# Kernel optimization log

Hardware: AMD Instinct MI355X
Metric: run time of the kernel (lower is better)

The kernel has to match this reference:

```python
import jax, jax.numpy as jnp
import numpy as np

TWO_PI = 2.0 * np.pi


def interp_H_circular(coords, signal):
    """Circular linear interpolation over a uniform group grid.
    coords: [M, 1] angles; signal: [K, C]. Returns [M, C]."""
    K = signal.shape[0]
    step = TWO_PI / K
    t = jnp.mod(coords[:, 0], TWO_PI) / step          # [M]
    i0f = jnp.floor(t)
    frac = (t - i0f)[:, None]                          # [M, 1]
    i0 = i0f.astype(jnp.int32) % K
    i1 = (i0 + 1) % K
    return (1.0 - frac) * signal[i0] + frac * signal[i1]


def rotate_grid(angles, grid):
    """angles: [No]; grid: [ks, ks, 2] (x, y). Returns [No, ks, ks, 2]."""
    c, s = jnp.cos(angles), jnp.sin(angles)
    R = jnp.stack([jnp.stack([c, -s], -1), jnp.stack([s, c], -1)], -2)  # [No,2,2]
    return jnp.einsum('nij,hwj->nhwi', R, grid)


def bilinear_sample(img, grid):
    """img: [B, H, W]; grid: [B, h, w, 2] with (x, y) in [-1, 1].
    Zero padding outside, align_corners-style mapping. Returns [B, h, w]."""
    B, H, W = img.shape
    x = (grid[..., 0] + 1.0) * 0.5 * (W - 1)
    y = (grid[..., 1] + 1.0) * 0.5 * (H - 1)
    x0f, y0f = jnp.floor(x), jnp.floor(y)
    wx, wy = x - x0f, y - y0f
    x0, y0 = x0f.astype(jnp.int32), y0f.astype(jnp.int32)
    b = jnp.arange(B)[:, None, None]

    def gather(yy, xx):
        valid = (yy >= 0) & (yy < H) & (xx >= 0) & (xx < W)
        v = img[b, jnp.clip(yy, 0, H - 1), jnp.clip(xx, 0, W - 1)]
        return jnp.where(valid, v, 0.0)

    return ((1 - wy) * (1 - wx) * gather(y0, x0)
            + (1 - wy) * wx * gather(y0, x0 + 1)
            + wy * (1 - wx) * gather(y0 + 1, x0)
            + wy * wx * gather(y0 + 1, x0 + 1))


def setup_inputs() -> dict:
    key = jax.random.key(0)
    k1, k2, k3, k4 = jax.random.split(key, 4)
    O, CIN, K, KS, NI, NO = 512, 512, 16, 7, 16, 16
    in_H = jax.random.uniform(k1, (NI, 1), dtype=jnp.float32) * TWO_PI
    out_H = jax.random.uniform(k2, (NO, 1), dtype=jnp.float32) * TWO_PI
    weight_H = jax.random.normal(k3, (O, CIN, K), dtype=jnp.float32) * 0.05
    weight = jax.random.normal(k4, (O, 1, KS, KS), dtype=jnp.float32) * 0.05
    grid_H = (jnp.arange(K, dtype=jnp.float32) * (TWO_PI / K)).reshape(K, 1)
    lin = jnp.linspace(-1.0, 1.0, KS, dtype=jnp.float32)
    gx, gy = jnp.meshgrid(lin, lin, indexing='xy')
    grid_Rn = jnp.stack([gx, gy], axis=-1)  # [KS, KS, 2]
    mask = jnp.ones((KS, KS), dtype=jnp.float32)
    return {"in_H": in_H, "out_H": out_H, "weight_H": weight_H,
            "weight": weight, "grid_H": grid_H, "grid_Rn": grid_Rn,
            "mask": mask}


def reference(in_H, out_H, weight_H, weight, grid_H, grid_Rn, mask):
    NI, NO = in_H.shape[0], out_H.shape[0]
    O, CIN_G, K = weight_H.shape
    KS = weight.shape[-1]

    out_H_inv = -out_H                                            # inverse_H
    # left_apply_to_H: pairwise group product -> [NI, NO, 1]
    H_prod_H = jnp.mod(in_H[:, None, :] + out_H_inv[None, :, :], TWO_PI)
    # left_apply_to_Rn: rotate spatial grid -> [NO, KS, KS, 2]
    H_prod_Rn = rotate_grid(out_H_inv[:, 0], grid_Rn)

    # interpolate_H over group grid of signal [K, CIN_G*O]
    sig = jnp.transpose(weight_H, (2, 1, 0)).reshape(K, -1)
    wH = interp_H_circular(H_prod_H.reshape(-1, 1), sig)          # [NI*NO, CIN_G*O]
    wH = wH.reshape(NI, NO, CIN_G, O)
    # .transpose(0,3).transpose(1,3) == permutation (3,0,2,1)
    weight_H_out = jnp.transpose(wH, (3, 0, 2, 1))                # [O, NI, CIN_G, NO]

    # interpolate_Rn: repeat_interleave kernels, tile rotated grids
    imgs = jnp.repeat(weight[:, 0], NO, axis=0)                   # [O*NO, KS, KS]
    grids = jnp.tile(H_prod_Rn, (O, 1, 1, 1))                     # [O*NO, KS, KS, 2]
    w = bilinear_sample(imgs, grids).reshape(O, NO, 1, KS, KS)
    w = mask * w                                                  # broadcast mask
    return (weight_H_out, w)
```

## Files before the change

### kernel.cpp

```cpp
#include <hip/hip_runtime.h>

#define TWO_PI_F 6.283185307179586f

#define C_O   512
#define C_CIN 512
#define C_K   16
#define C_KS  7
#define C_NI  16
#define C_NO  16

#define OUT0_SIZE (C_O * C_NI * C_CIN * C_NO)
#define OUT1_SIZE (C_O * C_NO * C_KS * C_KS)

#define SW_STRIDE 18

#define BILIN_PER_BLOCK 784

typedef float f32x4 __attribute__((ext_vector_type(4)));

__global__ __launch_bounds__(1024, 8) void fused_kernel(
    const float* __restrict__ in_H,
    const float* __restrict__ out_H,
    const float* __restrict__ weight_H,
    const float* __restrict__ weight,
    const float* __restrict__ grid_Rn,
    const float* __restrict__ mask,
    float* __restrict__ out0,
    float* __restrict__ out1)
{
    __shared__ float s_w[C_CIN * SW_STRIDE];
    __shared__ float s_t[C_NI * C_NO];

    const int tid = threadIdx.x;
    const int o   = blockIdx.x;

    if (tid < 256) {
        int ni = tid >> 4;
        int no = tid & 15;
        float x = in_H[ni] - out_H[no];
        float r = fmodf(x, TWO_PI_F);
        if (r < 0.0f) r += TWO_PI_F;
        s_t[tid] = r * (16.0f / TWO_PI_F);
    }

    const float4* wsrc = reinterpret_cast<const float4*>(weight_H) + (size_t)o * 2048;
#pragma unroll
    for (int j = 0; j < 2; ++j) {
        int f = j * 1024 + tid;
        float4 v = wsrc[f];
        int c    = f >> 2;
        int part = f & 3;
        float* row = &s_w[c * SW_STRIDE + part * 4];
        reinterpret_cast<float2*>(row)[0] = make_float2(v.x, v.y);
        reinterpret_cast<float2*>(row)[1] = make_float2(v.z, v.w);
        if (part == 0) s_w[c * SW_STRIDE + 16] = v.x;
    }
    __syncthreads();

    const int q    = tid & 3;
    const int crow = tid >> 2;
    const float* wv0 = &s_w[crow * SW_STRIDE];
    const float* wv1 = &s_w[(256 + crow) * SW_STRIDE];
    f32x4* obase = reinterpret_cast<f32x4*>(out0) + ((size_t)o << 15);

#pragma unroll
    for (int ni = 0; ni < C_NI; ++ni) {
        int   i0e[4];
        float fe[4];
#pragma unroll
        for (int e = 0; e < 4; ++e) {
            float tt = s_t[ni * 16 + q * 4 + e];
            float fl = floorf(tt);
            i0e[e] = ((int)fl) & 15;
            fe[e]  = tt - fl;
        }
#pragma unroll
        for (int half = 0; half < 2; ++half) {
            const float* wv = half ? wv1 : wv0;
            f32x4 res;
            res.x = (1.0f - fe[0]) * wv[i0e[0]] + fe[0] * wv[i0e[0] + 1];
            res.y = (1.0f - fe[1]) * wv[i0e[1]] + fe[1] * wv[i0e[1] + 1];
            res.z = (1.0f - fe[2]) * wv[i0e[2]] + fe[2] * wv[i0e[2] + 1];
            res.w = (1.0f - fe[3]) * wv[i0e[3]] + fe[3] * wv[i0e[3] + 1];
            __builtin_nontemporal_store(res, obase + ni * 2048 + half * 1024 + tid);
        }
    }

    if (tid < BILIN_PER_BLOCK) {
        int idx = o * BILIN_PER_BLOCK + tid;
        int pix = idx % 49;
        int no  = (idx / 49) & 15;
        int oo  = idx / (49 * 16);

        float gx = grid_Rn[pix * 2 + 0];
        float gy = grid_Rn[pix * 2 + 1];

        float ang = -out_H[no];
        float sn, cs;
        sincosf(ang, &sn, &cs);

        float x = cs * gx - sn * gy;
        float y = sn * gx + cs * gy;

        float X = (x + 1.0f) * 3.0f;
        float Y = (y + 1.0f) * 3.0f;

        float x0f = floorf(X), y0f = floorf(Y);
        float wx = X - x0f,    wy = Y - y0f;
        int   x0 = (int)x0f,   y0 = (int)y0f;

        const float* img = weight + oo * 49;

        auto gat = [&](int yy, int xx) -> float {
            bool v = (yy >= 0) & (yy < 7) & (xx >= 0) & (xx < 7);
            int yc = min(max(yy, 0), 6);
            int xc = min(max(xx, 0), 6);
            float val = img[yc * 7 + xc];
            return v ? val : 0.0f;
        };

        float r = (1.0f - wy) * (1.0f - wx) * gat(y0,     x0)
                + (1.0f - wy) * wx          * gat(y0,     x0 + 1)
                + wy          * (1.0f - wx) * gat(y0 + 1, x0)
                + wy          * wx          * gat(y0 + 1, x0 + 1);

        out1[idx] = mask[pix] * r;
    }
}

extern "C" void kernel_launch(void* const* d_in, const int* in_sizes, int n_in,
                              void* d_out, int out_size, void* d_ws, size_t ws_size,
                              hipStream_t stream) {
    const float* in_H     = (const float*)d_in[0];
    const float* out_H    = (const float*)d_in[1];
    const float* weight_H = (const float*)d_in[2];
    const float* weight   = (const float*)d_in[3];
    const float* grid_Rn  = (const float*)d_in[5];
    const float* mask     = (const float*)d_in[6];

    float* out0 = (float*)d_out;
    float* out1 = out0 + OUT0_SIZE;

    hipLaunchKernelGGL(fused_kernel, dim3(C_O), dim3(1024), 0, stream,
                       in_H, out_H, weight_H, weight, grid_Rn, mask, out0, out1);
}
```

Before: 59.04 us.

## Split work into finer blocks and separate bilinear blocks from interpolation blocks

Replaces the 512 blocks of 1024 threads with 784 dedicated bilinear-sampling blocks plus 4096 interpolation blocks of 512 threads. Each interpolation block handles one output channel, one half of the input channels and a group of four ni values, so it loads only a quarter of the angle table and half the weight row. The nontemporal store becomes a normal vector store. The aim is better load balance and occupancy across CUs for this write-bound kernel, at the cost of each weight row being reloaded four times and more launch blocks.

```diff
diff --git a/kernel.cpp b/kernel.cpp
--- a/kernel.cpp
+++ b/kernel.cpp
@@ -14,11 +14,12 @@
 
 #define SW_STRIDE 18
 
-#define BILIN_PER_BLOCK 784
+#define BILIN_BLOCKS  784
+#define INTERP_BLOCKS 4096
 
 typedef float f32x4 __attribute__((ext_vector_type(4)));
 
-__global__ __launch_bounds__(1024, 8) void fused_kernel(
+__global__ __launch_bounds__(512, 8) void fused_kernel(
     const float* __restrict__ in_H,
     const float* __restrict__ out_H,
     const float* __restrict__ weight_H,
@@ -28,69 +29,17 @@
     float* __restrict__ out0,
     float* __restrict__ out1)
 {
-    __shared__ float s_w[C_CIN * SW_STRIDE];
-    __shared__ float s_t[C_NI * C_NO];
+    __shared__ float s_w[256 * SW_STRIDE];
+    __shared__ float s_t[64];
 
     const int tid = threadIdx.x;
-    const int o   = blockIdx.x;
+    const int bid = blockIdx.x;
 
-    if (tid < 256) {
-        int ni = tid >> 4;
-        int no = tid & 15;
-        float x = in_H[ni] - out_H[no];
-        float r = fmodf(x, TWO_PI_F);
-        if (r < 0.0f) r += TWO_PI_F;
-        s_t[tid] = r * (16.0f / TWO_PI_F);
-    }
-
-    const float4* wsrc = reinterpret_cast<const float4*>(weight_H) + (size_t)o * 2048;
-#pragma unroll
-    for (int j = 0; j < 2; ++j) {
-        int f = j * 1024 + tid;
-        float4 v = wsrc[f];
-        int c    = f >> 2;
-        int part = f & 3;
-        float* row = &s_w[c * SW_STRIDE + part * 4];
-        reinterpret_cast<float2*>(row)[0] = make_float2(v.x, v.y);
-        reinterpret_cast<float2*>(row)[1] = make_float2(v.z, v.w);
-        if (part == 0) s_w[c * SW_STRIDE + 16] = v.x;
-    }
-    __syncthreads();
-
-    const int q    = tid & 3;
-    const int crow = tid >> 2;
-    const float* wv0 = &s_w[crow * SW_STRIDE];
-    const float* wv1 = &s_w[(256 + crow) * SW_STRIDE];
-    f32x4* obase = reinterpret_cast<f32x4*>(out0) + ((size_t)o << 15);
-
-#pragma unroll
-    for (int ni = 0; ni < C_NI; ++ni) {
-        int   i0e[4];
-        float fe[4];
-#pragma unroll
-        for (int e = 0; e < 4; ++e) {
-            float tt = s_t[ni * 16 + q * 4 + e];
-            float fl = floorf(tt);
-            i0e[e] = ((int)fl) & 15;
-            fe[e]  = tt - fl;
-        }
-#pragma unroll
-        for (int half = 0; half < 2; ++half) {
-            const float* wv = half ? wv1 : wv0;
-            f32x4 res;
-            res.x = (1.0f - fe[0]) * wv[i0e[0]] + fe[0] * wv[i0e[0] + 1];
-            res.y = (1.0f - fe[1]) * wv[i0e[1]] + fe[1] * wv[i0e[1] + 1];
-            res.z = (1.0f - fe[2]) * wv[i0e[2]] + fe[2] * wv[i0e[2] + 1];
-            res.w = (1.0f - fe[3]) * wv[i0e[3]] + fe[3] * wv[i0e[3] + 1];
-            __builtin_nontemporal_store(res, obase + ni * 2048 + half * 1024 + tid);
-        }
-    }
-
-    if (tid < BILIN_PER_BLOCK) {
-        int idx = o * BILIN_PER_BLOCK + tid;
+    if (bid < BILIN_BLOCKS) {
+        int idx = bid * 512 + tid;
         int pix = idx % 49;
         int no  = (idx / 49) & 15;
-        int oo  = idx / (49 * 16);
+        int o   = idx / (49 * 16);
 
         float gx = grid_Rn[pix * 2 + 0];
         float gy = grid_Rn[pix * 2 + 1];
@@ -109,7 +58,7 @@
         float wx = X - x0f,    wy = Y - y0f;
         int   x0 = (int)x0f,   y0 = (int)y0f;
 
-        const float* img = weight + oo * 49;
+        const float* img = weight + o * 49;
 
         auto gat = [&](int yy, int xx) -> float {
             bool v = (yy >= 0) & (yy < 7) & (xx >= 0) & (xx < 7);
@@ -125,6 +74,64 @@
                 + wy          * wx          * gat(y0 + 1, x0 + 1);
 
         out1[idx] = mask[pix] * r;
+        return;
+    }
+
+    const int ibid = bid - BILIN_BLOCKS;
+    const int o    = ibid >> 3;
+    const int ch   = (ibid >> 2) & 1;
+    const int nig  = ibid & 3;
+
+    if (tid < 64) {
+        int ni_l = tid >> 4;
+        int no   = tid & 15;
+        float x = in_H[nig * 4 + ni_l] - out_H[no];
+        float r = fmodf(x, TWO_PI_F);
+        if (r < 0.0f) r += TWO_PI_F;
+        s_t[tid] = r * (16.0f / TWO_PI_F);
+    }
+
+    const float4* wsrc = reinterpret_cast<const float4*>(weight_H)
+                       + (size_t)o * 2048 + ch * 1024;
+#pragma unroll
+    for (int j = 0; j < 2; ++j) {
+        int f = j * 512 + tid;
+        float4 v = wsrc[f];
+        int c    = f >> 2;
+        int part = f & 3;
+        float* row = &s_w[c * SW_STRIDE + part * 4];
+        reinterpret_cast<float2*>(row)[0] = make_float2(v.x, v.y);
+        reinterpret_cast<float2*>(row)[1] = make_float2(v.z, v.w);
+        if (part == 0) s_w[c * SW_STRIDE + 16] = v.x;
+    }
+    __syncthreads();
+
+    const int q    = tid & 3;
+    const int crow = tid >> 2;
+    f32x4* obase = reinterpret_cast<f32x4*>(out0)
+                 + ((size_t)((o << 4) + (nig << 2)) << 11) + (ch << 10);
+
+#pragma unroll
+    for (int ni_l = 0; ni_l < 4; ++ni_l) {
+        int   i0e[4];
+        float fe[4];
+#pragma unroll
+        for (int e = 0; e < 4; ++e) {
+            float tt = s_t[ni_l * 16 + q * 4 + e];
+            float fl = floorf(tt);
+            i0e[e] = ((int)fl) & 15;
+            fe[e]  = tt - fl;
+        }
+#pragma unroll
+        for (int half = 0; half < 2; ++half) {
+            const float* wv = &s_w[(half * 128 + crow) * SW_STRIDE];
+            f32x4 res;
+            res.x = (1.0f - fe[0]) * wv[i0e[0]] + fe[0] * wv[i0e[0] + 1];
+            res.y = (1.0f - fe[1]) * wv[i0e[1]] + fe[1] * wv[i0e[1] + 1];
+            res.z = (1.0f - fe[2]) * wv[i0e[2]] + fe[2] * wv[i0e[2] + 1];
+            res.w = (1.0f - fe[3]) * wv[i0e[3]] + fe[3] * wv[i0e[3] + 1];
+            obase[ni_l * 2048 + half * 512 + tid] = res;
+        }
     }
 }
 
@@ -141,6 +148,7 @@
     float* out0 = (float*)d_out;
     float* out1 = out0 + OUT0_SIZE;
 
-    hipLaunchKernelGGL(fused_kernel, dim3(C_O), dim3(1024), 0, stream,
+    hipLaunchKernelGGL(fused_kernel, dim3(BILIN_BLOCKS + INTERP_BLOCKS), dim3(512),
+                       0, stream,
                        in_H, out_H, weight_H, weight, grid_Rn, mask, out0, out1);
 }
```

Measured after the change: 55.02 us. 1.07x faster.
